# Kernel optimization log

Hardware: AMD Instinct MI355X
Metric: run time of the kernel (lower is better)

The kernel has to match this reference:

```python
import jax, jax.numpy as jnp
import numpy as np

H = 16        # num query heads
H_KV = 4      # num kv heads
D = 128       # head_dim
ROPE_BASE = 10000.0


def rotate_half(x):
    x1, x2 = jnp.split(x, 2, axis=-1)
    return jnp.concatenate((-x2, x1), axis=-1)


def rope_tables(T, d, dtype):
    inv_freq = 1.0 / (ROPE_BASE ** (np.arange(0, d, 2, dtype=np.float32) / d))
    t = np.arange(T, dtype=np.float32)
    freqs = np.outer(t, inv_freq)                 # [T, d/2]
    emb = np.concatenate((freqs, freqs), axis=-1)  # [T, d]
    return jnp.asarray(np.cos(emb), dtype), jnp.asarray(np.sin(emb), dtype)


def setup_inputs() -> dict:
    key = jax.random.key(0)
    ks = jax.random.split(key, 5)
    B, T, C = 2, 2048, 2048
    s = 0.02
    return {
        "x": jax.random.normal(ks[0], (B, T, C), jnp.float32),
        "wq": jax.random.normal(ks[1], (C, H * D), jnp.float32) * s,
        "wk": jax.random.normal(ks[2], (C, H_KV * D), jnp.float32) * s,
        "wv": jax.random.normal(ks[3], (C, H_KV * D), jnp.float32) * s,
        "wo": jax.random.normal(ks[4], (H * D, C), jnp.float32) * s,
    }


def reference(x, wq, wk, wv, wo):
    B, T, C = x.shape
    # QKV projections (bias=False); weights stored as [in, out]
    q = (x @ wq).reshape(B, T, H, D).transpose(0, 2, 1, 3)      # [B,H,T,D]
    k = (x @ wk).reshape(B, T, H_KV, D).transpose(0, 2, 1, 3)   # [B,Hkv,T,D]
    v = (x @ wv).reshape(B, T, H_KV, D).transpose(0, 2, 1, 3)
    # RoPE
    cos, sin = rope_tables(T, D, x.dtype)                        # [T,D]
    q = q * cos + rotate_half(q) * sin
    k = k * cos + rotate_half(k) * sin
    # GQA: repeat kv heads
    n_rep = H // H_KV
    k = jnp.repeat(k, n_rep, axis=1)                             # [B,H,T,D]
    v = jnp.repeat(v, n_rep, axis=1)
    # Causal SDPA
    scale = 1.0 / jnp.sqrt(jnp.asarray(D, x.dtype))
    att = jnp.einsum('bhqd,bhkd->bhqk', q, k) * scale            # [B,H,T,T]
    causal = jnp.tril(jnp.ones((T, T), dtype=bool))
    att = jnp.where(causal, att, jnp.asarray(-jnp.inf, x.dtype))
    att = jax.nn.softmax(att, axis=-1)
    y = jnp.einsum('bhqk,bhkd->bhqd', att, v)                    # [B,H,T,D]
    y = y.transpose(0, 2, 1, 3).reshape(B, T, H * D)
    return y @ wo
```

## Files before the change

### kernel.cpp

```cpp
#include <hip/hip_runtime.h>
#include <cstdint>
#include <cstddef>

typedef __attribute__((ext_vector_type(8))) short short8;
typedef __attribute__((ext_vector_type(4))) float f4;
typedef __attribute__((ext_vector_type(4))) unsigned int u4;

static __device__ __forceinline__ unsigned short f2bf(float x) {
  unsigned int u = __float_as_uint(x);
  unsigned int r = (u + 0x7FFFu + ((u >> 16) & 1u)) >> 16;
  return (unsigned short)r;
}

static __device__ __forceinline__ void gll16(const unsigned short* g, unsigned short* l) {
  __builtin_amdgcn_global_load_lds(
      (const __attribute__((address_space(1))) unsigned int*)g,
      (__attribute__((address_space(3))) unsigned int*)l, 16, 0, 0);
}

template <int N>
static __device__ __forceinline__ void wait_vmcnt() {
  if constexpr (N == 0) asm volatile("s_waitcnt vmcnt(0)" ::: "memory");
  else if constexpr (N == 1) asm volatile("s_waitcnt vmcnt(1)" ::: "memory");
  else if constexpr (N == 2) asm volatile("s_waitcnt vmcnt(2)" ::: "memory");
  else if constexpr (N == 3) asm volatile("s_waitcnt vmcnt(3)" ::: "memory");
  else if constexpr (N == 4) asm volatile("s_waitcnt vmcnt(4)" ::: "memory");
}

static __device__ __forceinline__ void trans_tile(
    const float* __restrict__ src, unsigned short* __restrict__ dst,
    int R, int C, int c0, int r0, int tid, unsigned short* tile) {
#pragma unroll
  for (int s = 0; s < 2; ++s) {
    int chunk = tid + s * 256;
    int c8 = chunk & 7, r = chunk >> 3;
    const float* p = src + (size_t)(r0 + r) * C + c0 + c8 * 8;
    f4 a = *(const f4*)p;
    f4 b = *(const f4*)(p + 4);
    union { unsigned short u[8]; u4 v; } pk;
#pragma unroll
    for (int i = 0; i < 4; ++i) { pk.u[i] = f2bf(a[i]); pk.u[4 + i] = f2bf(b[i]); }
    *(u4*)(tile + r * 72 + c8 * 8) = pk.v;
  }
  __syncthreads();
#pragma unroll
  for (int s = 0; s < 2; ++s) {
    int chunk = tid + s * 256;
    int r8 = chunk & 7, c = chunk >> 3;
    union { unsigned short u[8]; u4 v; } pk;
#pragma unroll
    for (int i = 0; i < 8; ++i) pk.u[i] = tile[(r8 * 8 + i) * 72 + c];
    *(u4*)(dst + (size_t)(c0 + c) * R + r0 + r8 * 8) = pk.v;
  }
}

__global__ __launch_bounds__(256) void k_prep(
    const float* __restrict__ x, const float* __restrict__ wq,
    const float* __restrict__ wk, const float* __restrict__ wv,
    unsigned short* __restrict__ Xb, unsigned short* __restrict__ WqkvT) {
  __shared__ alignas(16) unsigned short tile[64 * 72];
  int bid = blockIdx.x;
  int tid = threadIdx.x;
  if (bid < 4096) {
    int gid = bid * 256 + tid;
    const float* p = x + (size_t)gid * 8;
    f4 a = *(const f4*)p;
    f4 b = *(const f4*)(p + 4);
    union { unsigned short u[8]; u4 v; } pk;
#pragma unroll
    for (int i = 0; i < 4; ++i) { pk.u[i] = f2bf(a[i]); pk.u[4 + i] = f2bf(b[i]); }
    *(u4*)(Xb + (size_t)gid * 8) = pk.v;
  } else if (bid < 4096 + 1024) {
    int idx = bid - 4096;
    trans_tile(wq, WqkvT, 2048, 2048, (idx & 31) * 64, (idx >> 5) * 64, tid, tile);
  } else if (bid < 4096 + 1024 + 256) {
    int idx = bid - (4096 + 1024);
    trans_tile(wk, WqkvT + (size_t)2048 * 2048, 2048, 512,
               (idx & 7) * 64, (idx >> 3) * 64, tid, tile);
  } else {
    int idx = bid - (4096 + 1024 + 256);
    trans_tile(wv, WqkvT + (size_t)2560 * 2048, 2048, 512,
               (idx & 7) * 64, (idx >> 3) * 64, tid, tile);
  }
}

__global__ __launch_bounds__(256) void k_transpose_f(
    const float* __restrict__ src, unsigned short* __restrict__ dst, int R, int C) {
  __shared__ alignas(16) unsigned short tile[64 * 72];
  trans_tile(src, dst, R, C, blockIdx.x * 64, blockIdx.y * 64, threadIdx.x, tile);
}

#define PHASE(QM, QN, WAITC, ...)                                              \
  {                                                                            \
    wait_vmcnt<WAITC>();                                                       \
    __builtin_amdgcn_s_barrier();                                              \
    asm volatile("" ::: "memory");                                             \
    short8 af[FI][2], bf[2][2];                                                \
    _Pragma("unroll") for (int i = 0; i < FI; ++i)                             \
      _Pragma("unroll") for (int ks = 0; ks < 2; ++ks)                         \
        af[i][ks] = *(const short8*)(&As[cur][((QM) * (BM / 2) + wm * (BM / 4) + i * 16 + l16) * 64 + kswz[ks]]); \
    _Pragma("unroll") for (int j = 0; j < 2; ++j)                              \
      _Pragma("unroll") for (int ks = 0; ks < 2; ++ks)                         \
        bf[j][ks] = *(const short8*)(&Bs[cur][((QN) * 128 + wn * 32 + j * 16 + l16) * 64 + kswz[ks]]); \
    __VA_ARGS__                                                                \
    __builtin_amdgcn_s_setprio(1);                                             \
    _Pragma("unroll") for (int i = 0; i < FI; ++i)                             \
      _Pragma("unroll") for (int j = 0; j < 2; ++j)                            \
        _Pragma("unroll") for (int ks = 0; ks < 2; ++ks)                       \
          acc[(QM) * FI + i][(QN) * 2 + j] = __builtin_amdgcn_mfma_f32_16x16x32_bf16( \
              af[i][ks], bf[j][ks], acc[(QM) * FI + i][(QN) * 2 + j], 0, 0, 0); \
    __builtin_amdgcn_s_setprio(0);                                             \
  }

template <int BM, bool BF16OUT>
__global__ __launch_bounds__(512, 2) void k_gemm8(
    const unsigned short* __restrict__ A, const unsigned short* __restrict__ Bt,
    void* __restrict__ Cout, int M, int N, int K) {
  constexpr int CA = BM / 128;
  constexpr int FI = BM / 64;
  constexpr int WA = 2 + CA, WB = 2 * CA, WC = CA + 2, PB = CA;
  __shared__ alignas(16) unsigned short As[2][BM * 64];
  __shared__ alignas(16) unsigned short Bs[2][256 * 64];
  (void)M;

  int tid = threadIdx.x;
  int wid = tid >> 6, lane = tid & 63, quad = lane >> 4, l16 = lane & 15;
  int wm = wid >> 2, wn = wid & 3;

  int nx = gridDim.x;
  int id = blockIdx.y * nx + blockIdx.x;
  int nwg = nx * gridDim.y;
  int per = nwg >> 3;
  int lin = (id & 7) * per + (id >> 3);
  int bx = lin % nx, by = lin / nx;
  int bm = by * BM, bn = bx * 256;

  int srow = lane >> 3;
  int scol = ((lane & 7) ^ srow) << 3;
  const unsigned short* Ast = A + (size_t)(bm + wid * 8 + srow) * K + scol;
  const unsigned short* Bst = Bt + (size_t)(bn + wid * 8 + srow) * K + scol;
  const int ldsw = wid * 512;

  int kswz[2];
#pragma unroll
  for (int ks = 0; ks < 2; ++ks) kswz[ks] = (ks * 32 + quad * 8) ^ ((l16 & 7) << 3);

  f4 zero = {0.f, 0.f, 0.f, 0.f};
  f4 acc[2 * FI][4];
#pragma unroll
  for (int i = 0; i < 2 * FI; ++i)
#pragma unroll
    for (int j = 0; j < 4; ++j) acc[i][j] = zero;

  if constexpr (CA == 2) {
    gll16(Ast, &As[0][ldsw]);
    gll16(Ast + (size_t)64 * K, &As[0][ldsw + 64 * 64]);
  } else {
    gll16(Ast, &As[0][ldsw]);
  }
  gll16(Bst, &Bs[0][ldsw]);
  gll16(Bst + (size_t)64 * K, &Bs[0][ldsw + 64 * 64]);
  gll16(Bst + (size_t)128 * K, &Bs[0][ldsw + 128 * 64]);
  gll16(Bst + (size_t)192 * K, &Bs[0][ldsw + 192 * 64]);
  if constexpr (CA == 2) {
    gll16(Ast + (size_t)128 * K, &As[0][ldsw + 128 * 64]);
    gll16(Ast + (size_t)192 * K, &As[0][ldsw + 192 * 64]);
  } else {
    gll16(Ast + (size_t)64 * K, &As[0][ldsw + 64 * 64]);
  }

  int nt = K >> 6;
  int cur = 0;
  for (int t = 0; t < nt - 1; ++t) {
    int k0n = (t + 1) << 6;
    int nxt = cur ^ 1;
    unsigned short* Asn = &As[nxt][0];
    unsigned short* Bsn = &Bs[nxt][0];
    PHASE(0, 0, WA,
      if constexpr (CA == 2) {
        gll16(Ast + k0n, Asn + ldsw);
        gll16(Ast + (size_t)64 * K + k0n, Asn + ldsw + 64 * 64);
      } else {
        gll16(Ast + k0n, Asn + ldsw);
      })
    PHASE(0, 1, WB,
      gll16(Bst + k0n, Bsn + ldsw);
      gll16(Bst + (size_t)64 * K + k0n, Bsn + ldsw + 64 * 64);)
    PHASE(1, 0, WC,
      gll16(Bst + (size_t)128 * K + k0n, Bsn + ldsw + 128 * 64);
      gll16(Bst + (size_t)192 * K + k0n, Bsn + ldsw + 192 * 64);)
    PHASE(1, 1, -1,
      if constexpr (CA == 2) {
        gll16(Ast + (size_t)128 * K + k0n, Asn + ldsw + 128 * 64);
        gll16(Ast + (size_t)192 * K + k0n, Asn + ldsw + 192 * 64);
      } else {
        gll16(Ast + (size_t)64 * K + k0n, Asn + ldsw + 64 * 64);
      })
    cur = nxt;
  }
  PHASE(0, 0, WA, ;)
  PHASE(0, 1, PB, ;)
  PHASE(1, 0, 0, ;)
  PHASE(1, 1, -1, ;)

#pragma unroll
  for (int mi = 0; mi < 2 * FI; ++mi) {
    int row = bm + (mi / FI) * (BM / 2) + wm * (BM / 4) + (mi % FI) * 16 + quad * 4;
#pragma unroll
    for (int nj = 0; nj < 4; ++nj) {
      int col = bn + (nj >> 1) * 128 + wn * 32 + (nj & 1) * 16 + l16;
#pragma unroll
      for (int r = 0; r < 4; ++r) {
        if constexpr (BF16OUT)
          ((unsigned short*)Cout)[(size_t)(row + r) * N + col] = f2bf(acc[mi][nj][r]);
        else
          ((float*)Cout)[(size_t)(row + r) * N + col] = acc[mi][nj][r];
      }
    }
  }
}

__global__ __launch_bounds__(256) void k_ropev(
    unsigned short* __restrict__ QKV, unsigned short* __restrict__ VT) {
  __shared__ alignas(16) unsigned short tile[64 * 72];
  int bid = blockIdx.x;
  int tid = threadIdx.x;
  if (bid < 2560) {
    int gid = bid * 256 + tid;
    int c8 = gid & 7; int g = gid >> 3;
    int h20 = g % 20; g /= 20;
    int t = g & 2047; int b = g >> 11;
    bool isq = h20 < 16;
    size_t p = (size_t)(b * 2048 + t) * 3072 +
               (isq ? h20 * 128 : 2048 + (h20 - 16) * 128) + c8 * 8;
    short8 x0 = *(const short8*)(QKV + p);
    short8 x1 = *(const short8*)(QKV + p + 64);
    short8 o0, o1;
    float tf = (float)t;
#pragma unroll
    for (int i = 0; i < 8; ++i) {
      int d = c8 * 8 + i;
      float a0 = __uint_as_float((unsigned int)(unsigned short)x0[i] << 16);
      float a1 = __uint_as_float((unsigned int)(unsigned short)x1[i] << 16);
      float freq = exp2f(-(float)d * 0.20762050593046f);
      float ang = tf * freq;
      float cv = __cosf(ang), sv = __sinf(ang);
      float r0 = a0 * cv - a1 * sv;
      float r1 = a1 * cv + a0 * sv;
      if (isq) { r0 *= 0.088388347648318f; r1 *= 0.088388347648318f; }
      o0[i] = (short)f2bf(r0);
      o1[i] = (short)f2bf(r1);
    }
    *(short8*)(QKV + p) = o0;
    *(short8*)(QKV + p + 64) = o1;
  } else {
    int idx = bid - 2560;
    int t0 = (idx & 31) * 64;
    int g = idx >> 5;
    int dh = g & 1, hk = (g >> 1) & 3, b = g >> 3;
    int d0 = dh * 64;
    const unsigned short* src = QKV + (size_t)(b * 2048 + t0) * 3072 + 2560 + hk * 128 + d0;
#pragma unroll
    for (int s = 0; s < 2; ++s) {
      int chunk = tid + s * 256;
      int c8 = chunk & 7, r = chunk >> 3;
      *(u4*)(tile + r * 72 + c8 * 8) = *(const u4*)(src + (size_t)r * 3072 + c8 * 8);
    }
    __syncthreads();
    unsigned short* dst = VT + ((size_t)((b * 4 + hk) * 128 + d0)) * 2048 + t0;
#pragma unroll
    for (int s = 0; s < 2; ++s) {
      int chunk = tid + s * 256;
      int r8 = chunk & 7, c = chunk >> 3;
      union { unsigned short u[8]; u4 v; } pk;
#pragma unroll
      for (int i = 0; i < 8; ++i) pk.u[i] = tile[(r8 * 8 + i) * 72 + c];
      *(u4*)(dst + (size_t)c * 2048 + r8 * 8) = pk.v;
    }
  }
}

static __device__ __forceinline__ void attn_step(
    const unsigned short* __restrict__ Ks, const unsigned short* __restrict__ Vs,
    const short8* qf, f4* o, float& m, float& l,
    int quad, int l16, int qrow, int K0, bool mask, bool odd) {
  f4 zero = {0.f, 0.f, 0.f, 0.f};
  f4 st[4];
  __builtin_amdgcn_s_setprio(1);
#pragma unroll
  for (int kt = 0; kt < 4; ++kt) {
    st[kt] = zero;
#pragma unroll
    for (int ks = 0; ks < 4; ++ks) {
      short8 kf = *(const short8*)(Ks + (kt * 16 + l16) * 136 + ks * 32 + quad * 8);
      st[kt] = __builtin_amdgcn_mfma_f32_16x16x32_bf16(kf, qf[ks], st[kt], 0, 0, 0);
    }
  }
  __builtin_amdgcn_s_setprio(0);
  if (mask) {
#pragma unroll
    for (int kt = 0; kt < 4; ++kt)
#pragma unroll
      for (int r = 0; r < 4; ++r)
        if (K0 + kt * 16 + quad * 4 + r > qrow) st[kt][r] = -1e30f;
  }
  float sm = -1e30f;
#pragma unroll
  for (int kt = 0; kt < 4; ++kt)
#pragma unroll
    for (int r = 0; r < 4; ++r) sm = fmaxf(sm, st[kt][r]);
  sm = fmaxf(sm, __shfl_xor(sm, 16));
  sm = fmaxf(sm, __shfl_xor(sm, 32));
  bool grow = !__all(sm - m <= 8.f);
  float mnew = grow ? fmaxf(m, sm) : m;
  f4 pv[4];
  float rs = 0.f;
#pragma unroll
  for (int kt = 0; kt < 4; ++kt)
#pragma unroll
    for (int r = 0; r < 4; ++r) {
      pv[kt][r] = __expf(st[kt][r] - mnew);
      rs += pv[kt][r];
    }
  rs += __shfl_xor(rs, 16);
  rs += __shfl_xor(rs, 32);
  if (grow) {
    float alpha = __expf(m - mnew);
    l = l * alpha + rs;
    m = mnew;
#pragma unroll
    for (int i = 0; i < 8; ++i) o[i] *= alpha;
  } else {
    l += rs;
  }
  unsigned int c[4][2];
#pragma unroll
  for (int kt = 0; kt < 4; ++kt)
#pragma unroll
    for (int p = 0; p < 2; ++p)
      asm("v_cvt_pk_bf16_f32 %0, %1, %2"
          : "=v"(c[kt][p]) : "v"(pv[kt][2 * p]), "v"(pv[kt][2 * p + 1]));
#pragma unroll
  for (int kh = 0; kh < 2; ++kh) {
    unsigned int A0 = c[2 * kh][0], A1 = c[2 * kh][1];
    unsigned int B0 = c[2 * kh + 1][0], B1 = c[2 * kh + 1][1];
    asm("v_permlane32_swap_b32 %0, %1" : "+v"(A0), "+v"(B0));
    asm("v_permlane32_swap_b32 %0, %1" : "+v"(A1), "+v"(B1));
    unsigned int tA0 = (unsigned int)__builtin_amdgcn_ds_swizzle((int)A0, 0x401F);
    unsigned int tA1 = (unsigned int)__builtin_amdgcn_ds_swizzle((int)A1, 0x401F);
    unsigned int tB0 = (unsigned int)__builtin_amdgcn_ds_swizzle((int)B0, 0x401F);
    unsigned int tB1 = (unsigned int)__builtin_amdgcn_ds_swizzle((int)B1, 0x401F);
    union { unsigned int u[4]; short8 s; } pb;
    pb.u[0] = odd ? tB0 : A0;
    pb.u[1] = odd ? tB1 : A1;
    pb.u[2] = odd ? B0 : tA0;
    pb.u[3] = odd ? B1 : tA1;
    __builtin_amdgcn_s_setprio(1);
#pragma unroll
    for (int i = 0; i < 8; ++i) {
      short8 vf = *(const short8*)(Vs + (i * 16 + l16) * 72 + kh * 32 + quad * 8);
      o[i] = __builtin_amdgcn_mfma_f32_16x16x32_bf16(vf, pb.s, o[i], 0, 0, 0);
    }
    __builtin_amdgcn_s_setprio(0);
  }
}

__global__ __launch_bounds__(256, 2) void k_attn(
    const unsigned short* __restrict__ QKV,
    const unsigned short* __restrict__ VT,
    unsigned short* __restrict__ Y) {
  __shared__ alignas(16) unsigned short Ks[2][64 * 136];
  __shared__ alignas(16) unsigned short Vs[2][128 * 72];
  int tid = threadIdx.x;
  int w = tid >> 6, lane = tid & 63, quad = lane >> 4, l16 = lane & 15;
  bool odd = (quad & 1) != 0;
  int bh = blockIdx.y; int b = bh >> 4, h = bh & 15, hk = h >> 2;
  int v = blockIdx.x;
  int q0A = v * 64 + w * 16;
  int q0B = (31 - v) * 64 + w * 16;
  const unsigned short* Qh = QKV + (size_t)b * 2048 * 3072 + h * 128;
  const unsigned short* Kh = QKV + (size_t)b * 2048 * 3072 + 2048 + hk * 128;
  const unsigned short* Vh = VT + ((size_t)(b * 4 + hk) * 128) * 2048;

  int rK0 = tid >> 4, cK = tid & 15;
  int rV0 = tid >> 3, cV = tid & 7;

  short8 qfA[4], qfB[4];
#pragma unroll
  for (int ks = 0; ks < 4; ++ks) {
    qfA[ks] = *(const short8*)(Qh + (size_t)(q0A + l16) * 3072 + ks * 32 + quad * 8);
    qfB[ks] = *(const short8*)(Qh + (size_t)(q0B + l16) * 3072 + ks * 32 + quad * 8);
  }

  f4 zero = {0.f, 0.f, 0.f, 0.f};
  f4 oA[8], oB[8];
#pragma unroll
  for (int i = 0; i < 8; ++i) { oA[i] = zero; oB[i] = zero; }
  float mA = -1e30f, lA = 0.f, mB = -1e30f, lB = 0.f;

  int nch = 32 - v;

#pragma unroll
  for (int s = 0; s < 4; ++s) {
    int rK = rK0 + 16 * s;
    *(u4*)(&Ks[0][0] + rK * 136 + cK * 8) =
        *(const u4*)(Kh + (size_t)rK * 3072 + cK * 8);
    int rV = rV0 + 32 * s;
    *(u4*)(&Vs[0][0] + rV * 72 + cV * 8) =
        *(const u4*)(Vh + (size_t)rV * 2048 + cV * 8);
  }
  __syncthreads();

  for (int kc = 0; kc < nch; ++kc) {
    int cur = kc & 1, nxt = cur ^ 1;
    int K0 = kc * 64;
    bool have_next = (kc + 1) < nch;
    u4 kreg[4], vreg[4];
    if (have_next) {
      int K0n = K0 + 64;
#pragma unroll
      for (int s = 0; s < 4; ++s) {
        int rK = rK0 + 16 * s;
        kreg[s] = *(const u4*)(Kh + (size_t)(K0n + rK) * 3072 + cK * 8);
        int rV = rV0 + 32 * s;
        vreg[s] = *(const u4*)(Vh + (size_t)rV * 2048 + K0n + cV * 8);
      }
    }

    if (kc <= v)
      attn_step(&Ks[cur][0], &Vs[cur][0], qfA, oA, mA, lA, quad, l16, q0A + l16, K0, kc == v, odd);
    attn_step(&Ks[cur][0], &Vs[cur][0], qfB, oB, mB, lB, quad, l16, q0B + l16, K0, kc == nch - 1, odd);

    if (have_next) {
#pragma unroll
      for (int s = 0; s < 4; ++s) {
        int rK = rK0 + 16 * s;
        *(u4*)(&Ks[nxt][0] + rK * 136 + cK * 8) = kreg[s];
        int rV = rV0 + 32 * s;
        *(u4*)(&Vs[nxt][0] + rV * 72 + cV * 8) = vreg[s];
      }
    }
    __syncthreads();
  }

  float rA = 1.f / lA, rB = 1.f / lB;
  size_t yrowA = (size_t)(b * 2048 + q0A + l16) * 2048 + h * 128;
  size_t yrowB = (size_t)(b * 2048 + q0B + l16) * 2048 + h * 128;
#pragma unroll
  for (int i = 0; i < 8; ++i)
#pragma unroll
    for (int r = 0; r < 4; ++r) {
      Y[yrowA + i * 16 + quad * 4 + r] = f2bf(oA[i][r] * rA);
      Y[yrowB + i * 16 + quad * 4 + r] = f2bf(oB[i][r] * rB);
    }
}

extern "C" void kernel_launch(void* const* d_in, const int* in_sizes, int n_in,
                              void* d_out, int out_size, void* d_ws, size_t ws_size,
                              hipStream_t stream) {
  const float* x  = (const float*)d_in[0];
  const float* wq = (const float*)d_in[1];
  const float* wk = (const float*)d_in[2];
  const float* wv = (const float*)d_in[3];
  const float* wo = (const float*)d_in[4];
  float* outp = (float*)d_out;

  unsigned short* WqkvT = (unsigned short*)d_out;
  unsigned short* VT    = WqkvT + (size_t)3072 * 2048;
  unsigned short* Xb    = VT + (size_t)2 * 4 * 128 * 2048;
  unsigned short* QKV = (unsigned short*)d_ws;
  unsigned short* Yb  = QKV + (size_t)4096 * 3072;
  unsigned short* WoT = QKV;

  dim3 blk(256);
  k_prep<<<dim3(5632), blk, 0, stream>>>(x, wq, wk, wv, Xb, WqkvT);

  k_gemm8<256, true><<<dim3(12, 16), dim3(512), 0, stream>>>(
      Xb, WqkvT, QKV, 4096, 3072, 2048);

  k_ropev<<<dim3(3072), blk, 0, stream>>>(QKV, VT);

  k_attn<<<dim3(16, 32), blk, 0, stream>>>(QKV, VT, Yb);

  k_transpose_f<<<dim3(32, 32), blk, 0, stream>>>(wo, WoT, 2048, 2048);
  k_gemm8<128, false><<<dim3(8, 32), dim3(512), 0, stream>>>(
      Yb, WoT, outp, 4096, 2048, 2048);
}
```

Before: 303.5 us.

## Fuse Q RoPE into attention kernel and interleave PV MFMAs for both tiles

Q RoPE and the softmax scale are now applied to the Q fragments held in registers inside the attention kernel, so the RoPE/V-transpose kernel only rotates K and launches fewer blocks. This removes a full read-modify-write pass over Q in global memory. The attention step is also split into QK+softmax and PV phases. When both query tiles are active, their PV MFMAs are interleaved so each V fragment is loaded from LDS once for two MFMAs. The cost is more registers held live in a kernel with a launch bound of 2, and a small per-block RoPE compute on Q.

```diff
diff --git a/kernel.cpp b/kernel.cpp
--- a/kernel.cpp
+++ b/kernel.cpp
@@ -225,14 +225,12 @@
   __shared__ alignas(16) unsigned short tile[64 * 72];
   int bid = blockIdx.x;
   int tid = threadIdx.x;
-  if (bid < 2560) {
+  if (bid < 512) {
     int gid = bid * 256 + tid;
     int c8 = gid & 7; int g = gid >> 3;
-    int h20 = g % 20; g /= 20;
+    int h4 = g & 3; g >>= 2;
     int t = g & 2047; int b = g >> 11;
-    bool isq = h20 < 16;
-    size_t p = (size_t)(b * 2048 + t) * 3072 +
-               (isq ? h20 * 128 : 2048 + (h20 - 16) * 128) + c8 * 8;
+    size_t p = (size_t)(b * 2048 + t) * 3072 + 2048 + h4 * 128 + c8 * 8;
     short8 x0 = *(const short8*)(QKV + p);
     short8 x1 = *(const short8*)(QKV + p + 64);
     short8 o0, o1;
@@ -245,16 +243,13 @@
       float freq = exp2f(-(float)d * 0.20762050593046f);
       float ang = tf * freq;
       float cv = __cosf(ang), sv = __sinf(ang);
-      float r0 = a0 * cv - a1 * sv;
-      float r1 = a1 * cv + a0 * sv;
-      if (isq) { r0 *= 0.088388347648318f; r1 *= 0.088388347648318f; }
-      o0[i] = (short)f2bf(r0);
-      o1[i] = (short)f2bf(r1);
+      o0[i] = (short)f2bf(a0 * cv - a1 * sv);
+      o1[i] = (short)f2bf(a1 * cv + a0 * sv);
     }
     *(short8*)(QKV + p) = o0;
     *(short8*)(QKV + p + 64) = o1;
   } else {
-    int idx = bid - 2560;
+    int idx = bid - 512;
     int t0 = (idx & 31) * 64;
     int g = idx >> 5;
     int dh = g & 1, hk = (g >> 1) & 3, b = g >> 3;
@@ -280,23 +275,9 @@
   }
 }
 
-static __device__ __forceinline__ void attn_step(
-    const unsigned short* __restrict__ Ks, const unsigned short* __restrict__ Vs,
-    const short8* qf, f4* o, float& m, float& l,
-    int quad, int l16, int qrow, int K0, bool mask, bool odd) {
-  f4 zero = {0.f, 0.f, 0.f, 0.f};
-  f4 st[4];
-  __builtin_amdgcn_s_setprio(1);
-#pragma unroll
-  for (int kt = 0; kt < 4; ++kt) {
-    st[kt] = zero;
-#pragma unroll
-    for (int ks = 0; ks < 4; ++ks) {
-      short8 kf = *(const short8*)(Ks + (kt * 16 + l16) * 136 + ks * 32 + quad * 8);
-      st[kt] = __builtin_amdgcn_mfma_f32_16x16x32_bf16(kf, qf[ks], st[kt], 0, 0, 0);
-    }
-  }
-  __builtin_amdgcn_s_setprio(0);
+static __device__ __forceinline__ void softmax_pack(
+    f4* st, f4* o, float& m, float& l,
+    int quad, int l16, int qrow, int K0, bool mask, bool odd, short8* pb) {
   if (mask) {
 #pragma unroll
     for (int kt = 0; kt < 4; ++kt)
@@ -350,19 +331,60 @@
     unsigned int tA1 = (unsigned int)__builtin_amdgcn_ds_swizzle((int)A1, 0x401F);
     unsigned int tB0 = (unsigned int)__builtin_amdgcn_ds_swizzle((int)B0, 0x401F);
     unsigned int tB1 = (unsigned int)__builtin_amdgcn_ds_swizzle((int)B1, 0x401F);
-    union { unsigned int u[4]; short8 s; } pb;
-    pb.u[0] = odd ? tB0 : A0;
-    pb.u[1] = odd ? tB1 : A1;
-    pb.u[2] = odd ? B0 : tA0;
-    pb.u[3] = odd ? B1 : tA1;
-    __builtin_amdgcn_s_setprio(1);
+    union { unsigned int u[4]; short8 s; } pk;
+    pk.u[0] = odd ? tB0 : A0;
+    pk.u[1] = odd ? tB1 : A1;
+    pk.u[2] = odd ? B0 : tA0;
+    pk.u[3] = odd ? B1 : tA1;
+    pb[kh] = pk.s;
+  }
+}
+
+static __device__ __forceinline__ void qk_softmax(
+    const unsigned short* __restrict__ Ks, const short8* qf, f4* o, float& m, float& l,
+    int quad, int l16, int qrow, int K0, bool mask, bool odd, short8* pb) {
+  f4 zero = {0.f, 0.f, 0.f, 0.f};
+  f4 st[4];
+  __builtin_amdgcn_s_setprio(1);
+#pragma unroll
+  for (int kt = 0; kt < 4; ++kt) {
+    st[kt] = zero;
+#pragma unroll
+    for (int ks = 0; ks < 4; ++ks) {
+      short8 kf = *(const short8*)(Ks + (kt * 16 + l16) * 136 + ks * 32 + quad * 8);
+      st[kt] = __builtin_amdgcn_mfma_f32_16x16x32_bf16(kf, qf[ks], st[kt], 0, 0, 0);
+    }
+  }
+  __builtin_amdgcn_s_setprio(0);
+  softmax_pack(st, o, m, l, quad, l16, qrow, K0, mask, odd, pb);
+}
+
+static __device__ __forceinline__ void pv_step(
+    const unsigned short* __restrict__ Vs, const short8* pb, f4* o, int quad, int l16) {
+  __builtin_amdgcn_s_setprio(1);
+#pragma unroll
+  for (int kh = 0; kh < 2; ++kh)
 #pragma unroll
     for (int i = 0; i < 8; ++i) {
       short8 vf = *(const short8*)(Vs + (i * 16 + l16) * 72 + kh * 32 + quad * 8);
-      o[i] = __builtin_amdgcn_mfma_f32_16x16x32_bf16(vf, pb.s, o[i], 0, 0, 0);
-    }
-    __builtin_amdgcn_s_setprio(0);
-  }
+      o[i] = __builtin_amdgcn_mfma_f32_16x16x32_bf16(vf, pb[kh], o[i], 0, 0, 0);
+    }
+  __builtin_amdgcn_s_setprio(0);
+}
+
+static __device__ __forceinline__ void pv_step2(
+    const unsigned short* __restrict__ Vs, const short8* pbA, const short8* pbB,
+    f4* oA, f4* oB, int quad, int l16) {
+  __builtin_amdgcn_s_setprio(1);
+#pragma unroll
+  for (int kh = 0; kh < 2; ++kh)
+#pragma unroll
+    for (int i = 0; i < 8; ++i) {
+      short8 vf = *(const short8*)(Vs + (i * 16 + l16) * 72 + kh * 32 + quad * 8);
+      oA[i] = __builtin_amdgcn_mfma_f32_16x16x32_bf16(vf, pbA[kh], oA[i], 0, 0, 0);
+      oB[i] = __builtin_amdgcn_mfma_f32_16x16x32_bf16(vf, pbB[kh], oB[i], 0, 0, 0);
+    }
+  __builtin_amdgcn_s_setprio(0);
 }
 
 __global__ __launch_bounds__(256, 2) void k_attn(
@@ -391,6 +413,24 @@
     qfA[ks] = *(const short8*)(Qh + (size_t)(q0A + l16) * 3072 + ks * 32 + quad * 8);
     qfB[ks] = *(const short8*)(Qh + (size_t)(q0B + l16) * 3072 + ks * 32 + quad * 8);
   }
+#pragma unroll
+  for (int tix = 0; tix < 2; ++tix) {
+    short8* qf = tix ? qfB : qfA;
+    float tf = (float)((tix ? q0B : q0A) + l16);
+#pragma unroll
+    for (int ks = 0; ks < 2; ++ks)
+#pragma unroll
+      for (int i = 0; i < 8; ++i) {
+        int d = ks * 32 + quad * 8 + i;
+        float x0 = __uint_as_float((unsigned int)(unsigned short)qf[ks][i] << 16);
+        float x1 = __uint_as_float((unsigned int)(unsigned short)qf[ks + 2][i] << 16);
+        float freq = exp2f(-(float)d * 0.20762050593046f);
+        float ang = tf * freq;
+        float cv = __cosf(ang), sv = __sinf(ang);
+        qf[ks][i] = (short)f2bf((x0 * cv - x1 * sv) * 0.088388347648318f);
+        qf[ks + 2][i] = (short)f2bf((x1 * cv + x0 * sv) * 0.088388347648318f);
+      }
+  }
 
   f4 zero = {0.f, 0.f, 0.f, 0.f};
   f4 oA[8], oB[8];
@@ -427,9 +467,16 @@
       }
     }
 
-    if (kc <= v)
-      attn_step(&Ks[cur][0], &Vs[cur][0], qfA, oA, mA, lA, quad, l16, q0A + l16, K0, kc == v, odd);
-    attn_step(&Ks[cur][0], &Vs[cur][0], qfB, oB, mB, lB, quad, l16, q0B + l16, K0, kc == nch - 1, odd);
+    if (kc <= v) {
+      short8 pbA[2], pbB[2];
+      qk_softmax(&Ks[cur][0], qfA, oA, mA, lA, quad, l16, q0A + l16, K0, kc == v, odd, pbA);
+      qk_softmax(&Ks[cur][0], qfB, oB, mB, lB, quad, l16, q0B + l16, K0, false, odd, pbB);
+      pv_step2(&Vs[cur][0], pbA, pbB, oA, oB, quad, l16);
+    } else {
+      short8 pb[2];
+      qk_softmax(&Ks[cur][0], qfB, oB, mB, lB, quad, l16, q0B + l16, K0, kc == nch - 1, odd, pb);
+      pv_step(&Vs[cur][0], pb, oB, quad, l16);
+    }
 
     if (have_next) {
 #pragma unroll
@@ -478,7 +525,7 @@
   k_gemm8<256, true><<<dim3(12, 16), dim3(512), 0, stream>>>(
       Xb, WqkvT, QKV, 4096, 3072, 2048);
 
-  k_ropev<<<dim3(3072), blk, 0, stream>>>(QKV, VT);
+  k_ropev<<<dim3(1024), blk, 0, stream>>>(QKV, VT);
 
   k_attn<<<dim3(16, 32), blk, 0, stream>>>(QKV, VT, Yb);
 
```

Result: no change. 306.4 us (+0.9%).

## Fuse Q RoPE into attention kernel and single-buffer V tile in LDS

Applied to the files above, without the earlier changes.

Moves the RoPE rotation and softmax scaling of Q out of the separate ropev kernel and into the attention kernel's Q-fragment load, so ropev now only rotates K and transposes V. This removes one read-modify-write pass over the Q part of QKV. The V shared-memory tile is reduced from double to single buffering, with an extra barrier before it is overwritten. That lowers LDS use, possibly to improve occupancy, but adds a sync and serialises V staging with compute.

```diff
diff --git a/kernel.cpp b/kernel.cpp
--- a/kernel.cpp
+++ b/kernel.cpp
@@ -225,14 +225,12 @@
   __shared__ alignas(16) unsigned short tile[64 * 72];
   int bid = blockIdx.x;
   int tid = threadIdx.x;
-  if (bid < 2560) {
+  if (bid < 512) {
     int gid = bid * 256 + tid;
     int c8 = gid & 7; int g = gid >> 3;
-    int h20 = g % 20; g /= 20;
+    int h4 = g & 3; g >>= 2;
     int t = g & 2047; int b = g >> 11;
-    bool isq = h20 < 16;
-    size_t p = (size_t)(b * 2048 + t) * 3072 +
-               (isq ? h20 * 128 : 2048 + (h20 - 16) * 128) + c8 * 8;
+    size_t p = (size_t)(b * 2048 + t) * 3072 + 2048 + h4 * 128 + c8 * 8;
     short8 x0 = *(const short8*)(QKV + p);
     short8 x1 = *(const short8*)(QKV + p + 64);
     short8 o0, o1;
@@ -245,16 +243,13 @@
       float freq = exp2f(-(float)d * 0.20762050593046f);
       float ang = tf * freq;
       float cv = __cosf(ang), sv = __sinf(ang);
-      float r0 = a0 * cv - a1 * sv;
-      float r1 = a1 * cv + a0 * sv;
-      if (isq) { r0 *= 0.088388347648318f; r1 *= 0.088388347648318f; }
-      o0[i] = (short)f2bf(r0);
-      o1[i] = (short)f2bf(r1);
+      o0[i] = (short)f2bf(a0 * cv - a1 * sv);
+      o1[i] = (short)f2bf(a1 * cv + a0 * sv);
     }
     *(short8*)(QKV + p) = o0;
     *(short8*)(QKV + p + 64) = o1;
   } else {
-    int idx = bid - 2560;
+    int idx = bid - 512;
     int t0 = (idx & 31) * 64;
     int g = idx >> 5;
     int dh = g & 1, hk = (g >> 1) & 3, b = g >> 3;
@@ -370,7 +365,7 @@
     const unsigned short* __restrict__ VT,
     unsigned short* __restrict__ Y) {
   __shared__ alignas(16) unsigned short Ks[2][64 * 136];
-  __shared__ alignas(16) unsigned short Vs[2][128 * 72];
+  __shared__ alignas(16) unsigned short Vs[128 * 72];
   int tid = threadIdx.x;
   int w = tid >> 6, lane = tid & 63, quad = lane >> 4, l16 = lane & 15;
   bool odd = (quad & 1) != 0;
@@ -391,6 +386,24 @@
     qfA[ks] = *(const short8*)(Qh + (size_t)(q0A + l16) * 3072 + ks * 32 + quad * 8);
     qfB[ks] = *(const short8*)(Qh + (size_t)(q0B + l16) * 3072 + ks * 32 + quad * 8);
   }
+#pragma unroll
+  for (int tix = 0; tix < 2; ++tix) {
+    short8* qf = tix ? qfB : qfA;
+    float tf = (float)((tix ? q0B : q0A) + l16);
+#pragma unroll
+    for (int ks = 0; ks < 2; ++ks)
+#pragma unroll
+      for (int i = 0; i < 8; ++i) {
+        int d = ks * 32 + quad * 8 + i;
+        float x0 = __uint_as_float((unsigned int)(unsigned short)qf[ks][i] << 16);
+        float x1 = __uint_as_float((unsigned int)(unsigned short)qf[ks + 2][i] << 16);
+        float freq = exp2f(-(float)d * 0.20762050593046f);
+        float ang = tf * freq;
+        float cv = __cosf(ang), sv = __sinf(ang);
+        qf[ks][i] = (short)f2bf((x0 * cv - x1 * sv) * 0.088388347648318f);
+        qf[ks + 2][i] = (short)f2bf((x1 * cv + x0 * sv) * 0.088388347648318f);
+      }
+  }
 
   f4 zero = {0.f, 0.f, 0.f, 0.f};
   f4 oA[8], oB[8];
@@ -406,7 +419,7 @@
     *(u4*)(&Ks[0][0] + rK * 136 + cK * 8) =
         *(const u4*)(Kh + (size_t)rK * 3072 + cK * 8);
     int rV = rV0 + 32 * s;
-    *(u4*)(&Vs[0][0] + rV * 72 + cV * 8) =
+    *(u4*)(Vs + rV * 72 + cV * 8) =
         *(const u4*)(Vh + (size_t)rV * 2048 + cV * 8);
   }
   __syncthreads();
@@ -428,16 +441,20 @@
     }
 
     if (kc <= v)
-      attn_step(&Ks[cur][0], &Vs[cur][0], qfA, oA, mA, lA, quad, l16, q0A + l16, K0, kc == v, odd);
-    attn_step(&Ks[cur][0], &Vs[cur][0], qfB, oB, mB, lB, quad, l16, q0B + l16, K0, kc == nch - 1, odd);
+      attn_step(&Ks[cur][0], Vs, qfA, oA, mA, lA, quad, l16, q0A + l16, K0, kc == v, odd);
+    attn_step(&Ks[cur][0], Vs, qfB, oB, mB, lB, quad, l16, q0B + l16, K0, kc == nch - 1, odd);
 
     if (have_next) {
 #pragma unroll
       for (int s = 0; s < 4; ++s) {
         int rK = rK0 + 16 * s;
         *(u4*)(&Ks[nxt][0] + rK * 136 + cK * 8) = kreg[s];
+      }
+      __syncthreads();
+#pragma unroll
+      for (int s = 0; s < 4; ++s) {
         int rV = rV0 + 32 * s;
-        *(u4*)(&Vs[nxt][0] + rV * 72 + cV * 8) = vreg[s];
+        *(u4*)(Vs + rV * 72 + cV * 8) = vreg[s];
       }
     }
     __syncthreads();
@@ -478,7 +495,7 @@
   k_gemm8<256, true><<<dim3(12, 16), dim3(512), 0, stream>>>(
       Xb, WqkvT, QKV, 4096, 3072, 2048);
 
-  k_ropev<<<dim3(3072), blk, 0, stream>>>(QKV, VT);
+  k_ropev<<<dim3(1024), blk, 0, stream>>>(QKV, VT);
 
   k_attn<<<dim3(16, 32), blk, 0, stream>>>(QKV, VT, Yb);
 
```

Measured after the change: 294.4 us. -3.0%, faster.
